# Optimization experiments

Hardware: AMD Instinct MI355X
Metric: run time of the kernel (lower is better)

The kernel has to match this reference:

```python
import jax, jax.numpy as jnp
import numpy as np

N, D, K, ITERS = 500000, 64, 256, 10


def setup_inputs() -> dict:
    key = jax.random.key(0)
    k1, k2 = jax.random.split(key)
    x = jax.random.normal(k1, (N, D), dtype=jnp.float32)
    init_idx = jax.random.randint(k2, (K,), 0, N, dtype=jnp.int32)
    return {"x": x, "init_idx": init_idx, "n_clusters": K, "n_iters": ITERS}


def _lloyd_step(x, x_sq, centroids):
    dists = x_sq[:, None] - 2.0 * (x @ centroids.T) + jnp.sum(centroids * centroids, axis=1)[None, :]
    assign = jnp.argmin(dists, axis=1)                       # [N]
    sums = jax.ops.segment_sum(x, assign, num_segments=centroids.shape[0])   # [K, D]
    counts = jax.ops.segment_sum(jnp.ones((x.shape[0],), x.dtype), assign,
                                 num_segments=centroids.shape[0])            # [K]
    new_c = sums / jnp.maximum(counts, 1.0)[:, None]
    # empty clusters keep their previous centroid (sklearn relocates; carry-over is the standard Lloyd fallback)
    return jnp.where(counts[:, None] > 0, new_c, centroids)


def reference(x, init_idx, n_clusters, n_iters):
    # original: x.detach() -> no gradient flows through k-means
    x = jax.lax.stop_gradient(x)
    x_sq = jnp.sum(x * x, axis=1)  # [N], reused every iteration
    centroids0 = x[init_idx]       # [K, D] random-point init

    def body(c, _):
        return _lloyd_step(x, x_sq, c), None

    centroids, _ = jax.lax.scan(body, centroids0, None, length=n_iters)
    return centroids  # cluster_centers_ [K, D]
```

## Files before the change

### kernel.cpp

```cpp
#include <hip/hip_runtime.h>


#define D 64
#define K 256
#define ITERS 10
#define BLOCK 512
#define NB_MAX 256
#define EPS 2e-2f
#define PART_STRIDE (K * D + K)
#define SMEM_BYTES ((16384 + 16384) * 2 + (256 + 16384 + 256) * 4)

typedef __attribute__((ext_vector_type(8))) short bf16x8;
typedef __attribute__((ext_vector_type(4))) float f32x4;
typedef __attribute__((ext_vector_type(4))) short short4v;

__device__ __forceinline__ unsigned short f2bf(float f) {
    unsigned u = __builtin_bit_cast(unsigned, f);
    u = u + 0x7FFFu + ((u >> 16) & 1u);
    return (unsigned short)(u >> 16);
}
__device__ __forceinline__ float bf2f(unsigned short h) {
    unsigned u = ((unsigned)h) << 16;
    return __builtin_bit_cast(float, u);
}

__global__ void init_gather(const float* __restrict__ x,
                            const int* __restrict__ idx,
                            float* __restrict__ cent,
                            float* __restrict__ csq) {
    int k = blockIdx.x;
    int d = threadIdx.x;
    float v = x[(size_t)idx[k] * D + d];
    cent[k * D + d] = v;
    float s = v * v;
    #pragma unroll
    for (int off = 32; off > 0; off >>= 1) s += __shfl_down(s, off);
    if (d == 0) csq[k] = s;
}

__global__ __launch_bounds__(BLOCK, 1) void assign_mfma(
        const float* __restrict__ x,
        const float* __restrict__ cent,
        const float* __restrict__ csq_g,
        float* __restrict__ parts,
        int N, int ppb) {
    extern __shared__ char smem[];
    short* chi = (short*)smem;
    short* clo = chi + 16384;
    float* s_csq = (float*)(clo + 16384);
    float* s_sums = s_csq + 256;
    float* s_cnt = s_sums + 16384;

    const int tid = threadIdx.x;

    for (int i = tid; i < (K * D) / 4; i += BLOCK) {
        float4 c4 = ((const float4*)cent)[i];
        int elem = i * 4;
        int m = elem >> 6;
        int k0 = elem & 63;
        int g = k0 >> 3, e0 = k0 & 7;
        float cv[4] = {c4.x, c4.y, c4.z, c4.w};
        short4v hv, lv;
        #pragma unroll
        for (int j = 0; j < 4; ++j) {
            float v = -2.0f * cv[j];
            unsigned short h = f2bf(v);
            hv[j] = (short)h;
            lv[j] = (short)f2bf(v - bf2f(h));
        }
        int dst = (g * 256 + m) * 8 + e0;
        *(short4v*)&chi[dst] = hv;
        *(short4v*)&clo[dst] = lv;
    }
    if (tid < K) s_csq[tid] = csq_g[tid];
    for (int i = tid; i < K * D; i += BLOCK) s_sums[i] = 0.0f;
    if (tid < K) s_cnt[tid] = 0.0f;
    __syncthreads();

    const int wv = tid >> 6;
    const int lane = tid & 63;
    const int c15 = lane & 15;
    const int g4 = lane >> 4;

    const int base = blockIdx.x * ppb;
    int lim = base + ppb;
    if (lim > N) lim = N;
    const int ngroups = (lim > base) ? ((lim - base + 15) >> 4) : 0;

    for (int grp = wv; grp < ngroups; grp += BLOCK / 64) {
        const int p0 = base + grp * 16;
        int prow = p0 + c15;
        int pr = (prow < lim) ? prow : (lim - 1);
        const float* xr = x + (size_t)pr * D;

        bf16x8 bh[2], bl[2];
        #pragma unroll
        for (int s = 0; s < 2; ++s) {
            const float4* xp4 = (const float4*)(xr + s * 32 + g4 * 8);
            float4 u0 = xp4[0], u1 = xp4[1];
            float xv[8] = {u0.x, u0.y, u0.z, u0.w, u1.x, u1.y, u1.z, u1.w};
            #pragma unroll
            for (int e = 0; e < 8; ++e) {
                unsigned short h = f2bf(xv[e]);
                bh[s][e] = (short)h;
                bl[s][e] = (short)f2bf(xv[e] - bf2f(h));
            }
        }

        f32x4 acc[16];
        #pragma unroll
        for (int t = 0; t < 16; ++t) {
            f32x4 z = {0.f, 0.f, 0.f, 0.f};
            acc[t] = z;
            #pragma unroll
            for (int s = 0; s < 2; ++s) {
                int ai = (((s * 4 + g4) * 256) + t * 16 + c15) * 8;
                bf16x8 ah = *(const bf16x8*)&chi[ai];
                bf16x8 al = *(const bf16x8*)&clo[ai];
                acc[t] = __builtin_amdgcn_mfma_f32_16x16x32_bf16(ah, bh[s], acc[t], 0, 0, 0);
                acc[t] = __builtin_amdgcn_mfma_f32_16x16x32_bf16(ah, bl[s], acc[t], 0, 0, 0);
                acc[t] = __builtin_amdgcn_mfma_f32_16x16x32_bf16(al, bh[s], acc[t], 0, 0, 0);
            }
        }

        float gmin = 3.4e38f;
        int gidx = 0;
        #pragma unroll
        for (int t = 0; t < 16; ++t) {
            f32x4 q = *(const f32x4*)&s_csq[t * 16 + (g4 << 2)];
            #pragma unroll
            for (int r = 0; r < 4; ++r) {
                float sc = acc[t][r] + q[r];
                int m = t * 16 + (g4 << 2) + r;
                if (sc < gmin) { gmin = sc; gidx = m; }
            }
        }
        #pragma unroll
        for (int off = 16; off <= 32; off <<= 1) {
            float so = __shfl_xor(gmin, off);
            int io = __shfl_xor(gidx, off);
            if (so < gmin || (so == gmin && io < gidx)) { gmin = so; gidx = io; }
        }

        unsigned long long cmask = 0;
        #pragma unroll
        for (int t = 0; t < 16; ++t) {
            f32x4 q = *(const f32x4*)&s_csq[t * 16 + (g4 << 2)];
            #pragma unroll
            for (int r = 0; r < 4; ++r) {
                float sc = acc[t][r] + q[r];
                if (sc <= gmin + EPS) cmask |= 1ull << (t * 4 + r);
            }
        }
        int nb_ = __popcll(cmask);
        nb_ += __shfl_xor(nb_, 16);
        nb_ += __shfl_xor(nb_, 32);

        int bk = gidx;
        if (__any(nb_ >= 2)) {
            float xsq = 0.0f;
            #pragma unroll
            for (int d = 0; d < D; ++d) xsq += xr[d] * xr[d];
            float eb = 3.4e38f;
            int em = 0x7fffffff;
            unsigned long long mm = cmask;
            while (mm) {
                int b = __ffsll((unsigned long long)mm) - 1;
                mm &= mm - 1;
                int m = ((b >> 2) << 4) + (g4 << 2) + (b & 3);
                const float* cr = cent + m * D;
                float dot = 0.0f;
                #pragma unroll
                for (int d4 = 0; d4 < D; d4 += 4) {
                    float4 c4 = *(const float4*)(cr + d4);
                    dot += c4.x * xr[d4 + 0];
                    dot += c4.y * xr[d4 + 1];
                    dot += c4.z * xr[d4 + 2];
                    dot += c4.w * xr[d4 + 3];
                }
                float es = xsq - 2.0f * dot + s_csq[m];
                if (es < eb || (es == eb && m < em)) { eb = es; em = m; }
            }
            #pragma unroll
            for (int off = 16; off <= 32; off <<= 1) {
                float so = __shfl_xor(eb, off);
                int io = __shfl_xor(em, off);
                if (so < eb || (so == eb && io < em)) { eb = so; em = io; }
            }
            bk = em;
        }

        #pragma unroll 1
        for (int i = 0; i < 16; ++i) {
            int p = p0 + i;
            if (p >= lim) break;
            int mk = __shfl(bk, i);
            float xv = x[(size_t)p * D + lane];
            atomicAdd(&s_sums[mk * D + lane], xv);
            if (lane == 0) atomicAdd(&s_cnt[mk], 1.0f);
        }
    }

    __syncthreads();
    float* part = parts + (size_t)blockIdx.x * PART_STRIDE;
    for (int i = tid; i < K * D; i += BLOCK) part[i] = s_sums[i];
    if (tid < K) part[K * D + tid] = s_cnt[tid];
}

__global__ void finalize2(float* __restrict__ cent,
                          const float* __restrict__ parts,
                          float* __restrict__ csq_g,
                          int nb) {
    __shared__ float tmp[4][64];
    __shared__ float tcnt[4];
    int k = blockIdx.x;
    int sl = threadIdx.x >> 6;
    int d = threadIdx.x & 63;
    float s = 0.0f, c = 0.0f;
    for (int b = sl; b < nb; b += 4) {
        const float* pb = parts + (size_t)b * PART_STRIDE;
        s += pb[k * D + d];
        c += pb[K * D + k];
    }
    tmp[sl][d] = s;
    if (d == 0) tcnt[sl] = c;
    __syncthreads();
    if (sl == 0) {
        float st = tmp[0][d] + tmp[1][d] + tmp[2][d] + tmp[3][d];
        float ct = tcnt[0] + tcnt[1] + tcnt[2] + tcnt[3];
        float oldc = cent[k * D + d];
        float nc = (ct > 0.0f) ? (st / ct) : oldc;
        cent[k * D + d] = nc;
        float v = nc * nc;
        #pragma unroll
        for (int off = 32; off > 0; off >>= 1) v += __shfl_down(v, off);
        if (d == 0) csq_g[k] = v;
    }
}

extern "C" void kernel_launch(void* const* d_in, const int* in_sizes, int n_in,
                              void* d_out, int out_size, void* d_ws, size_t ws_size,
                              hipStream_t stream) {
    const float* x = (const float*)d_in[0];
    const int* init_idx = (const int*)d_in[1];

    int N = in_sizes[0] / D;

    float* cent = (float*)d_out;

    int nb = NB_MAX;
    size_t need = ((size_t)NB_MAX * PART_STRIDE + K) * sizeof(float);
    if (ws_size < need) {
        size_t avail = (ws_size > (size_t)K * sizeof(float))
                           ? ws_size - (size_t)K * sizeof(float) : 0;
        nb = (int)(avail / (PART_STRIDE * sizeof(float)));
        if (nb < 1) nb = 1;
    }
    float* parts = (float*)d_ws;
    float* csq = parts + (size_t)nb * PART_STRIDE;

    hipFuncSetAttribute(reinterpret_cast<const void*>(assign_mfma),
                        hipFuncAttributeMaxDynamicSharedMemorySize, SMEM_BYTES);

    init_gather<<<dim3(K), dim3(64), 0, stream>>>(x, init_idx, cent, csq);

    int ppb = (N + nb - 1) / nb;
    for (int it = 0; it < ITERS; ++it) {
        assign_mfma<<<dim3(nb), dim3(BLOCK), SMEM_BYTES, stream>>>(
            x, cent, csq, parts, N, ppb);
        finalize2<<<dim3(K), dim3(256), 0, stream>>>(cent, parts, csq, nb);
    }
}
```

Before: 2.569 ms.

## Process two point groups per wave, reuse loaded x for padded LDS accumulation

Each wave now handles two 16-point groups per iteration, sharing each centroid LDS fragment load across two MFMA accumulator sets and interleaving independent MFMA chains. The scatter step reuses the x values already held in registers instead of reloading each point row from global memory, and accumulates into a padded shared sums array (stride 66) to reduce bank conflicts. This raises register pressure by doubling the accumulators and the x buffers, and the per-lane atomics now hit 16 scattered addresses instead of one coalesced row.

```diff
diff --git a/kernel.cpp b/kernel.cpp
--- a/kernel.cpp
+++ b/kernel.cpp
@@ -7,8 +7,9 @@
 #define BLOCK 512
 #define NB_MAX 256
 #define EPS 2e-2f
+#define SPAD 66
 #define PART_STRIDE (K * D + K)
-#define SMEM_BYTES ((16384 + 16384) * 2 + (256 + 16384 + 256) * 4)
+#define SMEM_BYTES (32768 * 2 + (256 + 256 * SPAD + 256) * 4)
 
 typedef __attribute__((ext_vector_type(8))) short bf16x8;
 typedef __attribute__((ext_vector_type(4))) float f32x4;
@@ -38,6 +39,78 @@
     if (d == 0) csq[k] = s;
 }
 
+__device__ __forceinline__ int resolve_bk(
+        const f32x4 (&acc)[16], const float* __restrict__ s_csq,
+        const float* __restrict__ cent, const float* __restrict__ xr,
+        int g4) {
+    float gmin = 3.4e38f;
+    int gidx = 0;
+    #pragma unroll
+    for (int t = 0; t < 16; ++t) {
+        f32x4 q = *(const f32x4*)&s_csq[t * 16 + (g4 << 2)];
+        #pragma unroll
+        for (int r = 0; r < 4; ++r) {
+            float sc = acc[t][r] + q[r];
+            int m = t * 16 + (g4 << 2) + r;
+            if (sc < gmin) { gmin = sc; gidx = m; }
+        }
+    }
+    #pragma unroll
+    for (int off = 16; off <= 32; off <<= 1) {
+        float so = __shfl_xor(gmin, off);
+        int io = __shfl_xor(gidx, off);
+        if (so < gmin || (so == gmin && io < gidx)) { gmin = so; gidx = io; }
+    }
+    unsigned long long cmask = 0;
+    #pragma unroll
+    for (int t = 0; t < 16; ++t) {
+        f32x4 q = *(const f32x4*)&s_csq[t * 16 + (g4 << 2)];
+        #pragma unroll
+        for (int r = 0; r < 4; ++r) {
+            float sc = acc[t][r] + q[r];
+            if (sc <= gmin + EPS) cmask |= 1ull << (t * 4 + r);
+        }
+    }
+    int nb_ = __popcll(cmask);
+    nb_ += __shfl_xor(nb_, 16);
+    nb_ += __shfl_xor(nb_, 32);
+
+    int bk = gidx;
+    if (__any(nb_ >= 2)) {
+        float xsq = 0.0f;
+        #pragma unroll
+        for (int d = 0; d < D; ++d) xsq += xr[d] * xr[d];
+        float eb = 3.4e38f;
+        int em = 0x7fffffff;
+        unsigned long long mm = cmask;
+        while (mm) {
+            int b = __ffsll((unsigned long long)mm) - 1;
+            mm &= mm - 1;
+            int m = ((b >> 2) << 4) + (g4 << 2) + (b & 3);
+            const float* cr = cent + m * D;
+            float dot = 0.0f;
+            #pragma unroll
+            for (int d4 = 0; d4 < D; d4 += 4) {
+                float4 c4 = *(const float4*)(cr + d4);
+                dot += c4.x * xr[d4 + 0];
+                dot += c4.y * xr[d4 + 1];
+                dot += c4.z * xr[d4 + 2];
+                dot += c4.w * xr[d4 + 3];
+            }
+            float es = xsq - 2.0f * dot + s_csq[m];
+            if (es < eb || (es == eb && m < em)) { eb = es; em = m; }
+        }
+        #pragma unroll
+        for (int off = 16; off <= 32; off <<= 1) {
+            float so = __shfl_xor(eb, off);
+            int io = __shfl_xor(em, off);
+            if (so < eb || (so == eb && io < em)) { eb = so; em = io; }
+        }
+        bk = em;
+    }
+    return bk;
+}
+
 __global__ __launch_bounds__(BLOCK, 1) void assign_mfma(
         const float* __restrict__ x,
         const float* __restrict__ cent,
@@ -49,7 +122,7 @@
     short* clo = chi + 16384;
     float* s_csq = (float*)(clo + 16384);
     float* s_sums = s_csq + 256;
-    float* s_cnt = s_sums + 16384;
+    float* s_cnt = s_sums + 256 * SPAD;
 
     const int tid = threadIdx.x;
 
@@ -73,7 +146,7 @@
         *(short4v*)&clo[dst] = lv;
     }
     if (tid < K) s_csq[tid] = csq_g[tid];
-    for (int i = tid; i < K * D; i += BLOCK) s_sums[i] = 0.0f;
+    for (int i = tid; i < 256 * SPAD; i += BLOCK) s_sums[i] = 0.0f;
     if (tid < K) s_cnt[tid] = 0.0f;
     __syncthreads();
 
@@ -87,123 +160,103 @@
     if (lim > N) lim = N;
     const int ngroups = (lim > base) ? ((lim - base + 15) >> 4) : 0;
 
-    for (int grp = wv; grp < ngroups; grp += BLOCK / 64) {
-        const int p0 = base + grp * 16;
-        int prow = p0 + c15;
-        int pr = (prow < lim) ? prow : (lim - 1);
-        const float* xr = x + (size_t)pr * D;
-
-        bf16x8 bh[2], bl[2];
+    #pragma unroll 1
+    for (int g0 = wv; g0 < ngroups; g0 += 16) {
+        const int gB = g0 + 8;
+        const bool hasB = (gB < ngroups);
+
+        int prA = base + g0 * 16 + c15;
+        int prB = base + gB * 16 + c15;
+        const bool vA = prA < lim;
+        const bool vB = hasB && (prB < lim);
+        const float* xrA = x + (size_t)(vA ? prA : (lim - 1)) * D;
+        const float* xrB = x + (size_t)(vB ? prB : (lim - 1)) * D;
+
+        float xfA[16], xfB[16];
+        bf16x8 bhA[2], blA[2], bhB[2], blB[2];
         #pragma unroll
         for (int s = 0; s < 2; ++s) {
-            const float4* xp4 = (const float4*)(xr + s * 32 + g4 * 8);
-            float4 u0 = xp4[0], u1 = xp4[1];
-            float xv[8] = {u0.x, u0.y, u0.z, u0.w, u1.x, u1.y, u1.z, u1.w};
+            const float4* pa = (const float4*)(xrA + s * 32 + g4 * 8);
+            float4 a0 = pa[0], a1 = pa[1];
+            xfA[s * 8 + 0] = a0.x; xfA[s * 8 + 1] = a0.y;
+            xfA[s * 8 + 2] = a0.z; xfA[s * 8 + 3] = a0.w;
+            xfA[s * 8 + 4] = a1.x; xfA[s * 8 + 5] = a1.y;
+            xfA[s * 8 + 6] = a1.z; xfA[s * 8 + 7] = a1.w;
+            const float4* pb = (const float4*)(xrB + s * 32 + g4 * 8);
+            float4 b0 = pb[0], b1 = pb[1];
+            xfB[s * 8 + 0] = b0.x; xfB[s * 8 + 1] = b0.y;
+            xfB[s * 8 + 2] = b0.z; xfB[s * 8 + 3] = b0.w;
+            xfB[s * 8 + 4] = b1.x; xfB[s * 8 + 5] = b1.y;
+            xfB[s * 8 + 6] = b1.z; xfB[s * 8 + 7] = b1.w;
+        }
+        #pragma unroll
+        for (int s = 0; s < 2; ++s) {
             #pragma unroll
             for (int e = 0; e < 8; ++e) {
-                unsigned short h = f2bf(xv[e]);
-                bh[s][e] = (short)h;
-                bl[s][e] = (short)f2bf(xv[e] - bf2f(h));
-            }
-        }
-
-        f32x4 acc[16];
+                float va = xfA[s * 8 + e];
+                unsigned short ha = f2bf(va);
+                bhA[s][e] = (short)ha;
+                blA[s][e] = (short)f2bf(va - bf2f(ha));
+                float vb = xfB[s * 8 + e];
+                unsigned short hb = f2bf(vb);
+                bhB[s][e] = (short)hb;
+                blB[s][e] = (short)f2bf(vb - bf2f(hb));
+            }
+        }
+
+        f32x4 accA[16], accB[16];
         #pragma unroll
         for (int t = 0; t < 16; ++t) {
             f32x4 z = {0.f, 0.f, 0.f, 0.f};
-            acc[t] = z;
+            accA[t] = z; accB[t] = z;
             #pragma unroll
             for (int s = 0; s < 2; ++s) {
                 int ai = (((s * 4 + g4) * 256) + t * 16 + c15) * 8;
                 bf16x8 ah = *(const bf16x8*)&chi[ai];
                 bf16x8 al = *(const bf16x8*)&clo[ai];
-                acc[t] = __builtin_amdgcn_mfma_f32_16x16x32_bf16(ah, bh[s], acc[t], 0, 0, 0);
-                acc[t] = __builtin_amdgcn_mfma_f32_16x16x32_bf16(ah, bl[s], acc[t], 0, 0, 0);
-                acc[t] = __builtin_amdgcn_mfma_f32_16x16x32_bf16(al, bh[s], acc[t], 0, 0, 0);
-            }
-        }
-
-        float gmin = 3.4e38f;
-        int gidx = 0;
-        #pragma unroll
-        for (int t = 0; t < 16; ++t) {
-            f32x4 q = *(const f32x4*)&s_csq[t * 16 + (g4 << 2)];
-            #pragma unroll
-            for (int r = 0; r < 4; ++r) {
-                float sc = acc[t][r] + q[r];
-                int m = t * 16 + (g4 << 2) + r;
-                if (sc < gmin) { gmin = sc; gidx = m; }
-            }
-        }
-        #pragma unroll
-        for (int off = 16; off <= 32; off <<= 1) {
-            float so = __shfl_xor(gmin, off);
-            int io = __shfl_xor(gidx, off);
-            if (so < gmin || (so == gmin && io < gidx)) { gmin = so; gidx = io; }
-        }
-
-        unsigned long long cmask = 0;
-        #pragma unroll
-        for (int t = 0; t < 16; ++t) {
-            f32x4 q = *(const f32x4*)&s_csq[t * 16 + (g4 << 2)];
-            #pragma unroll
-            for (int r = 0; r < 4; ++r) {
-                float sc = acc[t][r] + q[r];
-                if (sc <= gmin + EPS) cmask |= 1ull << (t * 4 + r);
-            }
-        }
-        int nb_ = __popcll(cmask);
-        nb_ += __shfl_xor(nb_, 16);
-        nb_ += __shfl_xor(nb_, 32);
-
-        int bk = gidx;
-        if (__any(nb_ >= 2)) {
-            float xsq = 0.0f;
-            #pragma unroll
-            for (int d = 0; d < D; ++d) xsq += xr[d] * xr[d];
-            float eb = 3.4e38f;
-            int em = 0x7fffffff;
-            unsigned long long mm = cmask;
-            while (mm) {
-                int b = __ffsll((unsigned long long)mm) - 1;
-                mm &= mm - 1;
-                int m = ((b >> 2) << 4) + (g4 << 2) + (b & 3);
-                const float* cr = cent + m * D;
-                float dot = 0.0f;
+                accA[t] = __builtin_amdgcn_mfma_f32_16x16x32_bf16(ah, bhA[s], accA[t], 0, 0, 0);
+                accA[t] = __builtin_amdgcn_mfma_f32_16x16x32_bf16(ah, blA[s], accA[t], 0, 0, 0);
+                accA[t] = __builtin_amdgcn_mfma_f32_16x16x32_bf16(al, bhA[s], accA[t], 0, 0, 0);
+                accB[t] = __builtin_amdgcn_mfma_f32_16x16x32_bf16(ah, bhB[s], accB[t], 0, 0, 0);
+                accB[t] = __builtin_amdgcn_mfma_f32_16x16x32_bf16(ah, blB[s], accB[t], 0, 0, 0);
+                accB[t] = __builtin_amdgcn_mfma_f32_16x16x32_bf16(al, bhB[s], accB[t], 0, 0, 0);
+            }
+        }
+
+        {
+            int bk = resolve_bk(accA, s_csq, cent, xrA, g4);
+            if (vA) {
                 #pragma unroll
-                for (int d4 = 0; d4 < D; d4 += 4) {
-                    float4 c4 = *(const float4*)(cr + d4);
-                    dot += c4.x * xr[d4 + 0];
-                    dot += c4.y * xr[d4 + 1];
-                    dot += c4.z * xr[d4 + 2];
-                    dot += c4.w * xr[d4 + 3];
+                for (int s = 0; s < 2; ++s) {
+                    #pragma unroll
+                    for (int e = 0; e < 8; ++e)
+                        atomicAdd(&s_sums[bk * SPAD + s * 32 + g4 * 8 + e],
+                                  xfA[s * 8 + e]);
                 }
-                float es = xsq - 2.0f * dot + s_csq[m];
-                if (es < eb || (es == eb && m < em)) { eb = es; em = m; }
-            }
-            #pragma unroll
-            for (int off = 16; off <= 32; off <<= 1) {
-                float so = __shfl_xor(eb, off);
-                int io = __shfl_xor(em, off);
-                if (so < eb || (so == eb && io < em)) { eb = so; em = io; }
-            }
-            bk = em;
-        }
-
-        #pragma unroll 1
-        for (int i = 0; i < 16; ++i) {
-            int p = p0 + i;
-            if (p >= lim) break;
-            int mk = __shfl(bk, i);
-            float xv = x[(size_t)p * D + lane];
-            atomicAdd(&s_sums[mk * D + lane], xv);
-            if (lane == 0) atomicAdd(&s_cnt[mk], 1.0f);
+                if (g4 == 0) atomicAdd(&s_cnt[bk], 1.0f);
+            }
+        }
+        if (hasB) {
+            int bk = resolve_bk(accB, s_csq, cent, xrB, g4);
+            if (vB) {
+                #pragma unroll
+                for (int s = 0; s < 2; ++s) {
+                    #pragma unroll
+                    for (int e = 0; e < 8; ++e)
+                        atomicAdd(&s_sums[bk * SPAD + s * 32 + g4 * 8 + e],
+                                  xfB[s * 8 + e]);
+                }
+                if (g4 == 0) atomicAdd(&s_cnt[bk], 1.0f);
+            }
         }
     }
 
     __syncthreads();
     float* part = parts + (size_t)blockIdx.x * PART_STRIDE;
-    for (int i = tid; i < K * D; i += BLOCK) part[i] = s_sums[i];
+    for (int i = tid; i < K * D; i += BLOCK) {
+        int k = i >> 6, d = i & 63;
+        part[i] = s_sums[k * SPAD + d];
+    }
     if (tid < K) part[K * D + tid] = s_cnt[tid];
 }
 
```

New measurement: 2.433 ms. 5.3% less time.
